# Kernel tuning notes

Hardware: AMD Instinct MI355X
Metric: run time of the kernel (lower is better)

## Reference

```python
import jax, jax.numpy as jnp
import numpy as np

N, C, H, W = 32, 256, 56, 56   # batch, channels (inplanes == planes), spatial
EPS = 1e-5                     # BatchNorm eps (PyTorch default)
THR = 0.5                      # mask_hard_threshold (hard_inference mode)


def conv3x3(x, w):
    # stride 1, padding 1, no bias -- matches conv3x3() in the source
    return jax.lax.conv_general_dilated(
        x, w, window_strides=(1, 1), padding=((1, 1), (1, 1)),
        dimension_numbers=('NCHW', 'OIHW', 'NCHW'))


def bn_inf(y, g, b, mu, v):
    # inference-mode BatchNorm: per-channel affine with running stats
    s = (g * jax.lax.rsqrt(v + EPS))[None, :, None, None]
    return y * s + (b - mu * g * jax.lax.rsqrt(v + EPS))[None, :, None, None]


def setup_inputs() -> dict:
    key = jax.random.key(0)
    ks = jax.random.split(key, 10)
    x = jax.random.normal(ks[0], (N, C, H, W), jnp.float32)
    # main conv weights (3x3, no bias)
    w1 = jax.random.normal(ks[1], (C, C, 3, 3), jnp.float32) * 0.05
    w2 = jax.random.normal(ks[2], (C, C, 3, 3), jnp.float32) * 0.05
    # BN params (running stats)
    g1 = jnp.ones((C,), jnp.float32); b1 = jnp.zeros((C,), jnp.float32)
    mu1 = jax.random.normal(ks[3], (C,), jnp.float32) * 0.1
    v1 = jax.random.uniform(ks[4], (C,), jnp.float32, 0.5, 1.5)
    g2 = jnp.ones((C,), jnp.float32); b2 = jnp.zeros((C,), jnp.float32)
    mu2 = jax.random.normal(ks[5], (C,), jnp.float32) * 0.1
    v2 = jax.random.uniform(ks[6], (C,), jnp.float32, 0.5, 1.5)
    # mask convs: Conv2d(C, 1, 3, stride=1, pad=1) with bias; random weights so the
    wm1 = jax.random.normal(ks[7], (1, C, 3, 3), jnp.float32) * 0.05
    bm1 = jnp.zeros((1,), jnp.float32)
    wm2 = jax.random.normal(ks[8], (1, C, 3, 3), jnp.float32) * 0.05
    bm2 = jnp.zeros((1,), jnp.float32)
    return dict(x=x, w1=w1, w2=w2, g1=g1, b1=b1, mu1=mu1, v1=v1,
                g2=g2, b2=b2, mu2=mu2, v2=v2,
                wm1=wm1, bm1=bm1, wm2=wm2, bm2=bm2)


def reference(x, w1, w2, g1, b1, mu1, v1, g2, b2, mu2, v2, wm1, bm1, wm2, bm2):
    # Gumbel-Sigmoid gates in hard_inference mode: sigmoid(mask_conv(x)) > threshold.
    # [N,1,H,W] hard masks (non-differentiable constants w.r.t. the gate).
    m1 = (jax.nn.sigmoid(conv3x3(x, wm1) + bm1[None, :, None, None]) > THR).astype(x.dtype)
    m2 = (jax.nn.sigmoid(conv3x3(x, wm2) + bm2[None, :, None, None]) > THR).astype(x.dtype)
    # apply_proxy_dcn_bn_relu: gather patches at mask_loc -> matmul(W) -> BN -> ReLU
    # -> scatter (zeros elsewhere). Dense-equivalent: relu(bn(conv(x))) * mask.
    out = jax.nn.relu(bn_inf(conv3x3(x, w1), g1, b1, mu1, v1)) * m1
    # second conv: gather -> matmul -> BN -> scatter (ReLU applied after residual)
    out = bn_inf(conv3x3(out, w2), g2, b2, mu2, v2) * m2
    # residual add (identity: stride=1, inplanes==planes -> no downsample) + ReLU
    return jax.nn.relu(out + x)
```

## Files before the change

### kernel.cpp

```cpp
#include <hip/hip_runtime.h>
#include <hip/hip_bf16.h>


#define NB 32
#define C  256
#define H  56
#define W  56
#define HW (H*W)
#define NBHW (NB*HW)
#define EPSV 1e-5f
#define WELEM (C*C*9)
#define MSPL 2
#define MCH (C/MSPL)

typedef __hip_bfloat16 bf16;
typedef __attribute__((ext_vector_type(8))) short  bf16x8;
typedef __attribute__((ext_vector_type(4))) float  floatx4;

__global__ __launch_bounds__(128) void wcvt_kernel(
    const float* __restrict__ wm1, const float* __restrict__ wm2,
    double* __restrict__ wd)
{
    int i = blockIdx.x * 128 + threadIdx.x;
    if (i >= C * 18) return;
    int c = i / 18;
    int r = i - c * 18;
    int m = r / 9;
    int t = r - 9 * m;
    const float* src = m ? wm2 : wm1;
    wd[i] = (double)src[c * 9 + t];
}

__global__ __launch_bounds__(128) void mask_part_kernel(
    const float* __restrict__ x, const double* __restrict__ wd,
    double* __restrict__ z)
{
    int pixb  = blockIdx.x >> 1;
    int split = blockIdx.x & 1;
    int idx = pixb * 128 + threadIdx.x;
    int n  = idx / HW;
    int hw = idx - n * HW;

    const float*  xp = x  + (size_t)n * C * HW + (size_t)split * MCH * HW + hw;
    const double* wp = wd + (size_t)split * MCH * 18;

    double acc[18];
    #pragma unroll
    for (int j = 0; j < 18; ++j) acc[j] = 0.0;

    for (int c = 0; c < MCH; ++c) {
        double xv = (double)xp[(size_t)c * HW];
        const double* w = wp + c * 18;
        #pragma unroll
        for (int j = 0; j < 18; ++j)
            acc[j] += xv * w[j];
    }

    #pragma unroll
    for (int j = 0; j < 18; ++j)
        z[(size_t)(split * 18 + j) * NBHW + idx] = acc[j];
}

__global__ __launch_bounds__(256) void mask_reduce_kernel(
    const double* __restrict__ z,
    const float* __restrict__ bm1, const float* __restrict__ bm2,
    float* __restrict__ m1, float* __restrict__ m2)
{
    int idx = blockIdx.x * 256 + threadIdx.x;
    int n  = idx / HW;
    int hw = idx - n * HW;
    int h  = hw / W;
    int w_ = hw - h * W;

    double a1 = (double)bm1[0], a2 = (double)bm2[0];
    #pragma unroll
    for (int ky = 0; ky < 3; ++ky) {
        int y = h + ky - 1;
        if ((unsigned)y >= (unsigned)H) continue;
        #pragma unroll
        for (int kx = 0; kx < 3; ++kx) {
            int xx = w_ + kx - 1;
            if ((unsigned)xx >= (unsigned)W) continue;
            int t = ky * 3 + kx;
            size_t q = (size_t)n * HW + (size_t)y * W + xx;
            a1 += z[(size_t)(0 * 18 + 0 * 9 + t) * NBHW + q]
                + z[(size_t)(1 * 18 + 0 * 9 + t) * NBHW + q];
            a2 += z[(size_t)(0 * 18 + 1 * 9 + t) * NBHW + q]
                + z[(size_t)(1 * 18 + 1 * 9 + t) * NBHW + q];
        }
    }
    m1[idx] = (a1 > 0.0) ? 1.0f : 0.0f;
    m2[idx] = (a2 > 0.0) ? 1.0f : 0.0f;
}

__global__ __launch_bounds__(256) void transpose_kernel(
    const float* __restrict__ x, bf16* __restrict__ xb)
{
    __shared__ float tile[64][65];
    int bid = blockIdx.x;
    int pt = bid % 49; bid /= 49;
    int ct = bid % 4;  int n = bid / 4;
    int p0 = pt * 64, c0 = ct * 64;
    int tl = threadIdx.x & 63;
    int tg = threadIdx.x >> 6;
    const float* xp = x + ((size_t)(n*C + c0) * HW) + p0;
    #pragma unroll
    for (int i = 0; i < 16; ++i) {
        int cl = tg*16 + i;
        tile[cl][tl] = xp[(size_t)cl * HW + tl];
    }
    __syncthreads();
    bf16* op = xb + ((size_t)(n*HW + p0) * C) + c0;
    #pragma unroll
    for (int i = 0; i < 16; ++i) {
        int pl = tg*16 + i;
        op[(size_t)pl * C + tl] = __float2bfloat16(tile[tl][pl]);
    }
}

__global__ __launch_bounds__(256) void pack_kernel(
    const float* __restrict__ w1, const float* __restrict__ w2,
    bf16* __restrict__ w1p, bf16* __restrict__ w2p)
{
    int idx = blockIdx.x * 256 + threadIdx.x;
    const float* src = (idx < WELEM) ? w1 : w2;
    bf16* dst        = (idx < WELEM) ? w1p : w2p;
    int f = (idx < WELEM) ? idx : idx - WELEM;
    int e  = f & 7;
    int O  = f >> 3;
    int L  = O & 63;
    int j  = (O >> 6) & 15;
    int ks = (O >> 10) & 7;
    int t  = O >> 13;
    int co = j*16 + (L & 15);
    int ci = ks*32 + ((L >> 4) & 3)*8 + e;
    dst[f] = __float2bfloat16(src[((size_t)co*C + ci)*9 + t]);
}

template<bool FIRST>
__global__ __launch_bounds__(256, 2) void conv_mfma(
    const bf16* __restrict__ inb,
    const bf16* __restrict__ wp,
    const float* __restrict__ g,  const float* __restrict__ b,
    const float* __restrict__ mu, const float* __restrict__ vv,
    const float* __restrict__ mask,
    const float* __restrict__ xres,
    bf16* __restrict__ outb,
    float* __restrict__ outf)
{
    __shared__ uint4 patch4[3400];
    __shared__ float msk[128];
    short* patch = (short*)patch4;

    int tid = threadIdx.x;
    int L   = tid & 63;
    int wv  = tid >> 6;

    int t0g = blockIdx.x * 2;
    int n_s[2], y0_s[2], x0_s[2];
    size_t ibase_s[2];
    #pragma unroll
    for (int s = 0; s < 2; ++s) {
        int ts = t0g + s;
        int ns = ts / 49;
        int tl = ts - ns * 49;
        n_s[s]  = ns;
        y0_s[s] = (tl / 7) * 8;
        x0_s[s] = (tl % 7) * 8;
        ibase_s[s] = (size_t)ns * HW * C;
    }

    if (tid < 128) {
        int s  = tid >> 6;
        int p  = tid & 63;
        int pr = p >> 3, pc = p & 7;
        msk[tid] = mask[(size_t)n_s[s]*HW + (y0_s[s]+pr)*W + (x0_s[s]+pc)];
    }

    int m  = L & 15;
    int kb = L >> 4;
    int abase[8];
    #pragma unroll
    for (int mi = 0; mi < 8; ++mi) {
        int p   = mi*16 + m;
        int s   = p >> 6;
        int pl  = p & 63;
        int pos = (pl >> 3)*10 + (pl & 7);
        abase[mi] = s*13600 + pos*136 + kb*8;
    }

    floatx4 acc[8][4];
    #pragma unroll
    for (int mi = 0; mi < 8; ++mi)
        #pragma unroll
        for (int jj = 0; jj < 4; ++jj)
            acc[mi][jj] = (floatx4){0.f, 0.f, 0.f, 0.f};

    for (int ck = 0; ck < 2; ++ck) {
        if (ck) __syncthreads();
        for (int S = tid; S < 3200; S += 256) {
            int s   = S >= 1600;
            int r0  = S - s*1600;
            int q   = r0 & 15;
            int pos = r0 >> 4;
            int rr = pos / 10, cc = pos - (pos/10)*10;
            int y  = y0_s[s] + rr - 1;
            int xx = x0_s[s] + cc - 1;
            uint4 val = make_uint4(0u, 0u, 0u, 0u);
            if ((unsigned)y < (unsigned)H && (unsigned)xx < (unsigned)W)
                val = *(const uint4*)(inb + ibase_s[s] + (size_t)(y*W + xx)*C + ck*128 + q*8);
            patch4[s*1700 + pos*17 + q] = val;
        }
        __syncthreads();

        bf16x8 bcur[4], bnxt[4];
        bf16x8 acur[8], anxt[8];
        {
            int ks0 = ck*4;
            #pragma unroll
            for (int jj = 0; jj < 4; ++jj) {
                int jgl = wv*4 + jj;
                bcur[jj] = *(const bf16x8*)(wp + ((size_t)((0*8 + ks0)*16 + jgl)*64 + L)*8);
            }
            #pragma unroll
            for (int mi = 0; mi < 8; ++mi)
                acur[mi] = *(const bf16x8*)(patch + abase[mi]);
        }
        for (int gs = 0; gs < 36; ++gs) {
            if (gs < 35) {
                int g2 = gs + 1;
                int t2 = g2 >> 2, s2 = g2 & 3;
                int ks2 = ck*4 + s2;
                #pragma unroll
                for (int jj = 0; jj < 4; ++jj) {
                    int jgl = wv*4 + jj;
                    bnxt[jj] = *(const bf16x8*)(wp + ((size_t)((t2*8 + ks2)*16 + jgl)*64 + L)*8);
                }
                int ky2 = t2 / 3;
                int dt2 = ky2*10 + (t2 - ky2*3);
                int aoff2 = dt2*136 + s2*32;
                #pragma unroll
                for (int mi = 0; mi < 8; ++mi)
                    anxt[mi] = *(const bf16x8*)(patch + abase[mi] + aoff2);
            }
            #pragma unroll
            for (int mi = 0; mi < 8; ++mi)
                #pragma unroll
                for (int jj = 0; jj < 4; ++jj)
                    acc[mi][jj] = __builtin_amdgcn_mfma_f32_16x16x32_bf16(
                        acur[mi], bcur[jj], acc[mi][jj], 0, 0, 0);
            #pragma unroll
            for (int jj = 0; jj < 4; ++jj) bcur[jj] = bnxt[jj];
            #pragma unroll
            for (int mi = 0; mi < 8; ++mi) acur[mi] = anxt[mi];
        }
    }

    int quad  = L >> 4;
    int wbase = wv * 64;
    #pragma unroll
    for (int jj = 0; jj < 4; ++jj) {
        int co = wbase + jj*16 + (L & 15);
        float s_ = g[co] * rsqrtf(vv[co] + EPSV);
        float t_ = b[co] - mu[co] * s_;
        #pragma unroll
        for (int mi = 0; mi < 8; ++mi) {
            int pbase = mi*16 + quad*4;
            int s   = pbase >> 6;
            int pl  = pbase & 63;
            if (FIRST) {
                #pragma unroll
                for (int r = 0; r < 4; ++r) {
                    int p = pl + r;
                    float v = acc[mi][jj][r] * s_ + t_;
                    v = fmaxf(v, 0.f) * msk[pbase + r];
                    int pg = (y0_s[s] + (p >> 3))*W + (x0_s[s] + (p & 7));
                    outb[ibase_s[s] + (size_t)pg*C + co] = __float2bfloat16(v);
                }
            } else {
                int pg = (y0_s[s] + (pl >> 3))*W + (x0_s[s] + (pl & 7));
                size_t oidx = ((size_t)(n_s[s]*C + co))*HW + pg;
                floatx4 xr = *(const floatx4*)(xres + oidx);
                floatx4 ov;
                #pragma unroll
                for (int r = 0; r < 4; ++r) {
                    float v = acc[mi][jj][r] * s_ + t_;
                    v = v * msk[pbase + r] + xr[r];
                    ov[r] = fmaxf(v, 0.f);
                }
                *(floatx4*)(outf + oidx) = ov;
            }
        }
    }
}

extern "C" void kernel_launch(void* const* d_in, const int* in_sizes, int n_in,
                              void* d_out, int out_size, void* d_ws, size_t ws_size,
                              hipStream_t stream) {
    const float* x   = (const float*)d_in[0];
    const float* w1  = (const float*)d_in[1];
    const float* w2  = (const float*)d_in[2];
    const float* g1  = (const float*)d_in[3];
    const float* b1  = (const float*)d_in[4];
    const float* mu1 = (const float*)d_in[5];
    const float* v1  = (const float*)d_in[6];
    const float* g2  = (const float*)d_in[7];
    const float* b2  = (const float*)d_in[8];
    const float* mu2 = (const float*)d_in[9];
    const float* v2  = (const float*)d_in[10];
    const float* wm1 = (const float*)d_in[11];
    const float* bm1 = (const float*)d_in[12];
    const float* wm2 = (const float*)d_in[13];
    const float* bm2 = (const float*)d_in[14];
    float* out = (float*)d_out;

    float* m1   = (float*)d_ws;
    float* m2   = m1 + (size_t)NBHW;
    bf16*  w1p  = (bf16*)(m2 + (size_t)NBHW);
    bf16*  w2p  = w1p + WELEM;
    bf16*  tmpb = w2p + WELEM;
    double* z   = (double*)(tmpb + (size_t)NBHW*C);
    double* wd  = z + (size_t)MSPL*18*NBHW;
    bf16*  xb   = (bf16*)d_out;

    wcvt_kernel<<<(C*18 + 127)/128, 128, 0, stream>>>(wm1, wm2, wd);
    mask_part_kernel<<<(NBHW/128)*MSPL, 128, 0, stream>>>(x, wd, z);
    mask_reduce_kernel<<<NBHW/256, 256, 0, stream>>>(z, bm1, bm2, m1, m2);
    transpose_kernel<<<NB*4*49, 256, 0, stream>>>(x, xb);
    pack_kernel<<<2*WELEM/256, 256, 0, stream>>>(w1, w2, w1p, w2p);

    const int grid = NBHW / 128;
    conv_mfma<true ><<<grid, 256, 0, stream>>>(
        xb,   w1p, g1, b1, mu1, v1, m1, nullptr, tmpb, nullptr);
    conv_mfma<false><<<grid, 256, 0, stream>>>(
        tmpb, w2p, g2, b2, mu2, v2, m2, x, nullptr, out);
}
```

Baseline: 549.6 us.

## Split conv tile across 8 waves and remap block order

The conv kernel moves from 256 to 512 threads per block. Eight waves now each compute a 64-pixel by 64-channel sub-tile instead of four waves each covering 128 pixels, which halves the per-wave accumulators and cuts register pressure. Block IDs are remapped with an XCD-style swizzle to improve weight cache locality, and the inner loop is unrolled by four. Each weight fragment is now loaded by two waves instead of one, so global weight traffic per block doubles, and occupancy is limited to one block per launch bound.

```diff
diff --git a/kernel.cpp b/kernel.cpp
--- a/kernel.cpp
+++ b/kernel.cpp
@@ -138,7 +138,7 @@
 }
 
 template<bool FIRST>
-__global__ __launch_bounds__(256, 2) void conv_mfma(
+__global__ __launch_bounds__(512, 1) void conv_mfma(
     const bf16* __restrict__ inb,
     const bf16* __restrict__ wp,
     const float* __restrict__ g,  const float* __restrict__ b,
@@ -155,8 +155,13 @@
     int tid = threadIdx.x;
     int L   = tid & 63;
     int wv  = tid >> 6;
-
-    int t0g = blockIdx.x * 2;
+    int wr  = wv >> 2;
+    int wc  = wv & 3;
+
+    int bid = (int)blockIdx.x;
+    bid = (bid & 7) * 98 + (bid >> 3);
+
+    int t0g = bid * 2;
     int n_s[2], y0_s[2], x0_s[2];
     size_t ibase_s[2];
     #pragma unroll
@@ -179,26 +184,26 @@
 
     int m  = L & 15;
     int kb = L >> 4;
-    int abase[8];
-    #pragma unroll
-    for (int mi = 0; mi < 8; ++mi) {
+    int abase[4];
+    #pragma unroll
+    for (int mi = 0; mi < 4; ++mi) {
         int p   = mi*16 + m;
-        int s   = p >> 6;
-        int pl  = p & 63;
-        int pos = (pl >> 3)*10 + (pl & 7);
-        abase[mi] = s*13600 + pos*136 + kb*8;
-    }
-
-    floatx4 acc[8][4];
-    #pragma unroll
-    for (int mi = 0; mi < 8; ++mi)
+        int pos = (p >> 3)*10 + (p & 7);
+        abase[mi] = wr*13600 + pos*136 + kb*8;
+    }
+
+    const bf16* wpw = wp + (size_t)L*8 + (size_t)wc*4*512;
+
+    floatx4 acc[4][4];
+    #pragma unroll
+    for (int mi = 0; mi < 4; ++mi)
         #pragma unroll
         for (int jj = 0; jj < 4; ++jj)
             acc[mi][jj] = (floatx4){0.f, 0.f, 0.f, 0.f};
 
     for (int ck = 0; ck < 2; ++ck) {
         if (ck) __syncthreads();
-        for (int S = tid; S < 3200; S += 256) {
+        for (int S = tid; S < 3200; S += 512) {
             int s   = S >= 1600;
             int r0  = S - s*1600;
             int q   = r0 & 15;
@@ -214,37 +219,34 @@
         __syncthreads();
 
         bf16x8 bcur[4], bnxt[4];
-        bf16x8 acur[8], anxt[8];
+        bf16x8 acur[4], anxt[4];
         {
-            int ks0 = ck*4;
-            #pragma unroll
-            for (int jj = 0; jj < 4; ++jj) {
-                int jgl = wv*4 + jj;
-                bcur[jj] = *(const bf16x8*)(wp + ((size_t)((0*8 + ks0)*16 + jgl)*64 + L)*8);
-            }
-            #pragma unroll
-            for (int mi = 0; mi < 8; ++mi)
+            const bf16* bp = wpw + (size_t)(0*8 + ck*4) * 8192;
+            #pragma unroll
+            for (int jj = 0; jj < 4; ++jj)
+                bcur[jj] = *(const bf16x8*)(bp + jj*512);
+            #pragma unroll
+            for (int mi = 0; mi < 4; ++mi)
                 acur[mi] = *(const bf16x8*)(patch + abase[mi]);
         }
+        #pragma unroll 4
         for (int gs = 0; gs < 36; ++gs) {
             if (gs < 35) {
                 int g2 = gs + 1;
                 int t2 = g2 >> 2, s2 = g2 & 3;
-                int ks2 = ck*4 + s2;
-                #pragma unroll
-                for (int jj = 0; jj < 4; ++jj) {
-                    int jgl = wv*4 + jj;
-                    bnxt[jj] = *(const bf16x8*)(wp + ((size_t)((t2*8 + ks2)*16 + jgl)*64 + L)*8);
-                }
+                const bf16* bp = wpw + (size_t)(t2*8 + ck*4 + s2) * 8192;
+                #pragma unroll
+                for (int jj = 0; jj < 4; ++jj)
+                    bnxt[jj] = *(const bf16x8*)(bp + jj*512);
                 int ky2 = t2 / 3;
                 int dt2 = ky2*10 + (t2 - ky2*3);
                 int aoff2 = dt2*136 + s2*32;
                 #pragma unroll
-                for (int mi = 0; mi < 8; ++mi)
+                for (int mi = 0; mi < 4; ++mi)
                     anxt[mi] = *(const bf16x8*)(patch + abase[mi] + aoff2);
             }
             #pragma unroll
-            for (int mi = 0; mi < 8; ++mi)
+            for (int mi = 0; mi < 4; ++mi)
                 #pragma unroll
                 for (int jj = 0; jj < 4; ++jj)
                     acc[mi][jj] = __builtin_amdgcn_mfma_f32_16x16x32_bf16(
@@ -252,28 +254,26 @@
             #pragma unroll
             for (int jj = 0; jj < 4; ++jj) bcur[jj] = bnxt[jj];
             #pragma unroll
-            for (int mi = 0; mi < 8; ++mi) acur[mi] = anxt[mi];
+            for (int mi = 0; mi < 4; ++mi) acur[mi] = anxt[mi];
         }
     }
 
     int quad  = L >> 4;
-    int wbase = wv * 64;
+    int s     = wr;
     #pragma unroll
     for (int jj = 0; jj < 4; ++jj) {
-        int co = wbase + jj*16 + (L & 15);
+        int co = wc*64 + jj*16 + (L & 15);
         float s_ = g[co] * rsqrtf(vv[co] + EPSV);
         float t_ = b[co] - mu[co] * s_;
         #pragma unroll
-        for (int mi = 0; mi < 8; ++mi) {
-            int pbase = mi*16 + quad*4;
-            int s   = pbase >> 6;
-            int pl  = pbase & 63;
+        for (int mi = 0; mi < 4; ++mi) {
+            int pl = mi*16 + quad*4;
             if (FIRST) {
                 #pragma unroll
                 for (int r = 0; r < 4; ++r) {
                     int p = pl + r;
                     float v = acc[mi][jj][r] * s_ + t_;
-                    v = fmaxf(v, 0.f) * msk[pbase + r];
+                    v = fmaxf(v, 0.f) * msk[s*64 + p];
                     int pg = (y0_s[s] + (p >> 3))*W + (x0_s[s] + (p & 7));
                     outb[ibase_s[s] + (size_t)pg*C + co] = __float2bfloat16(v);
                 }
@@ -285,7 +285,7 @@
                 #pragma unroll
                 for (int r = 0; r < 4; ++r) {
                     float v = acc[mi][jj][r] * s_ + t_;
-                    v = v * msk[pbase + r] + xr[r];
+                    v = v * msk[s*64 + pl + r] + xr[r];
                     ov[r] = fmaxf(v, 0.f);
                 }
                 *(floatx4*)(outf + oidx) = ov;
@@ -330,8 +330,8 @@
     pack_kernel<<<2*WELEM/256, 256, 0, stream>>>(w1, w2, w1p, w2p);
 
     const int grid = NBHW / 128;
-    conv_mfma<true ><<<grid, 256, 0, stream>>>(
+    conv_mfma<true ><<<grid, 512, 0, stream>>>(
         xb,   w1p, g1, b1, mu1, v1, m1, nullptr, tmpb, nullptr);
-    conv_mfma<false><<<grid, 256, 0, stream>>>(
+    conv_mfma<false><<<grid, 512, 0, stream>>>(
         tmpb, w2p, g2, b2, mu2, v2, m2, x, nullptr, out);
 }
```

Result: slower. 684.1 us (+24.5%).

## Stream weights into LDS with async global_load_lds double buffering per tap

Applied to the files above, without the earlier changes.

Restructures the MFMA conv main loop. Input channels are now processed in 8 chunks of 32 with a smaller A patch, and each tap's weight tile is copied into double-buffered LDS with async global-to-LDS loads, instead of each wave loading its weights straight from global into registers. Block IDs are also remapped with a stride-8 swizzle to change the block-to-tile assignment across the grid. The change adds a __syncthreads per tap (72 per block) and shrinks K reuse per A stage, trading more barriers for less register pressure and coalesced weight staging.

```diff
diff --git a/kernel.cpp b/kernel.cpp
--- a/kernel.cpp
+++ b/kernel.cpp
@@ -16,6 +16,12 @@
 typedef __hip_bfloat16 bf16;
 typedef __attribute__((ext_vector_type(8))) short  bf16x8;
 typedef __attribute__((ext_vector_type(4))) float  floatx4;
+
+__device__ __forceinline__ void async_copy16(void* lds, const void* gptr) {
+    __builtin_amdgcn_global_load_lds(
+        (const __attribute__((address_space(1))) unsigned int*)gptr,
+        (__attribute__((address_space(3))) unsigned int*)lds, 16, 0, 0);
+}
 
 __global__ __launch_bounds__(128) void wcvt_kernel(
     const float* __restrict__ wm1, const float* __restrict__ wm2,
@@ -148,46 +154,52 @@
     bf16* __restrict__ outb,
     float* __restrict__ outf)
 {
-    __shared__ uint4 patch4[3400];
+    __shared__ uint4 albufq[800];
+    __shared__ uint4 bbufq[2][1024];
     __shared__ float msk[128];
-    short* patch = (short*)patch4;
+    short* albuf = (short*)albufq;
 
     int tid = threadIdx.x;
     int L   = tid & 63;
     int wv  = tid >> 6;
 
-    int t0g = blockIdx.x * 2;
-    int n_s[2], y0_s[2], x0_s[2];
-    size_t ibase_s[2];
-    #pragma unroll
-    for (int s = 0; s < 2; ++s) {
-        int ts = t0g + s;
-        int ns = ts / 49;
-        int tl = ts - ns * 49;
-        n_s[s]  = ns;
-        y0_s[s] = (tl / 7) * 8;
-        x0_s[s] = (tl % 7) * 8;
-        ibase_s[s] = (size_t)ns * HW * C;
-    }
+    int bid = (int)blockIdx.x;
+    bid = (bid & 7) * 98 + (bid >> 3);
+
+    int t0g = bid * 2;
+    int n0 = t0g / 49, tl0 = t0g - n0 * 49;
+    int y0a = (tl0 / 7) * 8, x0a = (tl0 % 7) * 8;
+    size_t ibasea = (size_t)n0 * HW * C;
+    int t1g = t0g + 1;
+    int n1 = t1g / 49, tl1 = t1g - n1 * 49;
+    int y0b = (tl1 / 7) * 8, x0b = (tl1 % 7) * 8;
+    size_t ibaseb = (size_t)n1 * HW * C;
 
     if (tid < 128) {
         int s  = tid >> 6;
         int p  = tid & 63;
         int pr = p >> 3, pc = p & 7;
-        msk[tid] = mask[(size_t)n_s[s]*HW + (y0_s[s]+pr)*W + (x0_s[s]+pc)];
+        int nn = s ? n1  : n0;
+        int yy = s ? y0b : y0a;
+        int xx = s ? x0b : x0a;
+        msk[tid] = mask[(size_t)nn*HW + (yy+pr)*W + (xx+pc)];
     }
 
     int m  = L & 15;
     int kb = L >> 4;
-    int abase[8];
+    int a_addr[8];
     #pragma unroll
     for (int mi = 0; mi < 8; ++mi) {
-        int p   = mi*16 + m;
-        int s   = p >> 6;
-        int pl  = p & 63;
-        int pos = (pl >> 3)*10 + (pl & 7);
-        abase[mi] = s*13600 + pos*136 + kb*8;
-    }
+        int p    = mi*16 + m;
+        int sub  = p >> 6;
+        int pl   = p & 63;
+        int pos2 = sub*100 + (pl >> 3)*10 + (pl & 7);
+        a_addr[mi] = (kb*200 + pos2) * 8;
+    }
+    int b_addr[4];
+    #pragma unroll
+    for (int jj = 0; jj < 4; ++jj)
+        b_addr[jj] = ((wv*4 + jj)*64 + L) * 8;
 
     floatx4 acc[8][4];
     #pragma unroll
@@ -196,67 +208,72 @@
         for (int jj = 0; jj < 4; ++jj)
             acc[mi][jj] = (floatx4){0.f, 0.f, 0.f, 0.f};
 
-    for (int ck = 0; ck < 2; ++ck) {
-        if (ck) __syncthreads();
-        for (int S = tid; S < 3200; S += 256) {
-            int s   = S >= 1600;
-            int r0  = S - s*1600;
-            int q   = r0 & 15;
-            int pos = r0 >> 4;
-            int rr = pos / 10, cc = pos - (pos/10)*10;
-            int y  = y0_s[s] + rr - 1;
-            int xx = x0_s[s] + cc - 1;
+    auto stageA = [&](int ck) {
+        for (int S = tid; S < 800; S += 256) {
+            int kbg  = S / 200;
+            int pos2 = S - kbg*200;
+            int sub  = pos2 >= 100;
+            int pos  = sub ? pos2 - 100 : pos2;
+            int r  = pos / 10;
+            int c  = pos - r*10;
+            int yy = (sub ? y0b : y0a) + r - 1;
+            int xx = (sub ? x0b : x0a) + c - 1;
             uint4 val = make_uint4(0u, 0u, 0u, 0u);
-            if ((unsigned)y < (unsigned)H && (unsigned)xx < (unsigned)W)
-                val = *(const uint4*)(inb + ibase_s[s] + (size_t)(y*W + xx)*C + ck*128 + q*8);
-            patch4[s*1700 + pos*17 + q] = val;
-        }
-        __syncthreads();
-
-        bf16x8 bcur[4], bnxt[4];
-        bf16x8 acur[8], anxt[8];
-        {
-            int ks0 = ck*4;
-            #pragma unroll
-            for (int jj = 0; jj < 4; ++jj) {
-                int jgl = wv*4 + jj;
-                bcur[jj] = *(const bf16x8*)(wp + ((size_t)((0*8 + ks0)*16 + jgl)*64 + L)*8);
+            if ((unsigned)yy < (unsigned)H && (unsigned)xx < (unsigned)W) {
+                size_t ib = sub ? ibaseb : ibasea;
+                val = *(const uint4*)(inb + ib + (size_t)(yy*W + xx)*C + ck*32 + kbg*8);
             }
+            albufq[S] = val;
+        }
+    };
+    auto issueB = [&](int tap, int ck, int buf) {
+        const bf16* src = wp + (size_t)(tap*8 + ck) * 8192;
+        short* dstb = (short*)bbufq[buf];
+        #pragma unroll
+        for (int i = 0; i < 4; ++i) {
+            int off = (wv*4 + i) * 512;
+            async_copy16(dstb + off, src + off + L*8);
+        }
+    };
+
+    stageA(0);
+    issueB(0, 0, 0);
+    __syncthreads();
+
+    int cur = 0;
+    for (int ck = 0; ck < 8; ++ck) {
+        #pragma unroll
+        for (int tap = 0; tap < 9; ++tap) {
+            if (tap < 8)          issueB(tap + 1, ck,     cur ^ 1);
+            else if (ck < 7)      issueB(0,       ck + 1, cur ^ 1);
+
+            const int ky = tap / 3;
+            const int aoff = (ky*10 + (tap - ky*3)) * 8;
+            short* bb = (short*)bbufq[cur];
+            bf16x8 af[8], bfr[4];
             #pragma unroll
             for (int mi = 0; mi < 8; ++mi)
-                acur[mi] = *(const bf16x8*)(patch + abase[mi]);
-        }
-        for (int gs = 0; gs < 36; ++gs) {
-            if (gs < 35) {
-                int g2 = gs + 1;
-                int t2 = g2 >> 2, s2 = g2 & 3;
-                int ks2 = ck*4 + s2;
-                #pragma unroll
-                for (int jj = 0; jj < 4; ++jj) {
-                    int jgl = wv*4 + jj;
-                    bnxt[jj] = *(const bf16x8*)(wp + ((size_t)((t2*8 + ks2)*16 + jgl)*64 + L)*8);
-                }
-                int ky2 = t2 / 3;
-                int dt2 = ky2*10 + (t2 - ky2*3);
-                int aoff2 = dt2*136 + s2*32;
-                #pragma unroll
-                for (int mi = 0; mi < 8; ++mi)
-                    anxt[mi] = *(const bf16x8*)(patch + abase[mi] + aoff2);
-            }
+                af[mi] = *(const bf16x8*)(albuf + a_addr[mi] + aoff);
+            #pragma unroll
+            for (int jj = 0; jj < 4; ++jj)
+                bfr[jj] = *(const bf16x8*)(bb + b_addr[jj]);
             #pragma unroll
             for (int mi = 0; mi < 8; ++mi)
                 #pragma unroll
                 for (int jj = 0; jj < 4; ++jj)
                     acc[mi][jj] = __builtin_amdgcn_mfma_f32_16x16x32_bf16(
-                        acur[mi], bcur[jj], acc[mi][jj], 0, 0, 0);
-            #pragma unroll
-            for (int jj = 0; jj < 4; ++jj) bcur[jj] = bnxt[jj];
-            #pragma unroll
-            for (int mi = 0; mi < 8; ++mi) acur[mi] = anxt[mi];
-        }
-    }
-
-    int quad  = L >> 4;
+                        af[mi], bfr[jj], acc[mi][jj], 0, 0, 0);
+
+            __syncthreads();
+            cur ^= 1;
+        }
+        if (ck < 7) {
+            stageA(ck + 1);
+            __syncthreads();
+        }
+    }
+
+    int quad = L >> 4;
     int wbase = wv * 64;
     #pragma unroll
     for (int jj = 0; jj < 4; ++jj) {
@@ -266,20 +283,24 @@
         #pragma unroll
         for (int mi = 0; mi < 8; ++mi) {
             int pbase = mi*16 + quad*4;
-            int s   = pbase >> 6;
-            int pl  = pbase & 63;
+            int sub   = pbase >> 6;
+            int pl    = pbase & 63;
+            int yy = sub ? y0b : y0a;
+            int xx = sub ? x0b : x0a;
+            size_t ib = sub ? ibaseb : ibasea;
+            int nn = sub ? n1 : n0;
             if (FIRST) {
                 #pragma unroll
                 for (int r = 0; r < 4; ++r) {
                     int p = pl + r;
                     float v = acc[mi][jj][r] * s_ + t_;
                     v = fmaxf(v, 0.f) * msk[pbase + r];
-                    int pg = (y0_s[s] + (p >> 3))*W + (x0_s[s] + (p & 7));
-                    outb[ibase_s[s] + (size_t)pg*C + co] = __float2bfloat16(v);
+                    int pg = (yy + (p >> 3))*W + (xx + (p & 7));
+                    outb[ib + (size_t)pg*C + co] = __float2bfloat16(v);
                 }
             } else {
-                int pg = (y0_s[s] + (pl >> 3))*W + (x0_s[s] + (pl & 7));
-                size_t oidx = ((size_t)(n_s[s]*C + co))*HW + pg;
+                int pg = (yy + (pl >> 3))*W + (xx + (pl & 7));
+                size_t oidx = ((size_t)(nn*C + co))*HW + pg;
                 floatx4 xr = *(const floatx4*)(xres + oidx);
                 floatx4 ov;
                 #pragma unroll
```

Result: slower. 603.1 us (+9.7%).
